# Kernel optimization log

Hardware: AMD Instinct MI355X
Metric: run time of the kernel (lower is better)

## Reference

```python
import jax, jax.numpy as jnp
import numpy as np

N, E, De, Dv = 40000, 8000, 32, 8   # nodes, hyperedges, edge degree, node degree
D, Q, EIG, VOC, NC = 256, 256, 64, 1000, 40  # vertex/edge dim, query dim, eig dim, centrality vocab, classes
LN_EPS = 1e-5


def _linear(x, W, b):
    return x @ W + b


def _layernorm(x, g, b):
    mu = jnp.mean(x, axis=-1, keepdims=True)
    var = jnp.mean(jnp.square(x - mu), axis=-1, keepdims=True)
    return (x - mu) * jax.lax.rsqrt(var + LN_EPS) * g + b


def setup_inputs() -> dict:
    key = jax.random.key(0)
    ks = iter(jax.random.split(key, 64))
    def nrm(shape, s=0.02):
        return (jax.random.normal(next(ks), shape, jnp.float32) * s).astype(jnp.float32)
    inp = {
        'vfeat': jax.random.normal(next(ks), (N, D), jnp.float32),
        'efeat': jax.random.normal(next(ks), (E, D), jnp.float32),
        'eign_vec': jax.random.normal(next(ks), (N, EIG), jnp.float32),
        'feat_v_gcn': jax.random.normal(next(ks), (N, D), jnp.float32),
        'cent1': jax.random.uniform(next(ks), (E, De), jnp.float32),
        'cent2': jax.random.uniform(next(ks), (N, Dv), jnp.float32),
        'cent_idx': jax.random.randint(next(ks), (N,), 0, VOC),
        'uniq_idx': jax.random.randint(next(ks), (N,), 0, VOC),
        'edge2node': jax.random.randint(next(ks), (E, De), 0, N),
        'node2edge': jax.random.randint(next(ks), (N, Dv), 0, E),
        # learned parameters (W: [in, out])
        'W_vtx': nrm((D, D)), 'b_vtx': jnp.zeros((D,), jnp.float32),
        'W_pe': nrm((EIG, D)), 'b_pe': jnp.zeros((D,), jnp.float32),
        'cs_emb': nrm((VOC, D)), 'un_emb': nrm((VOC, D)),
        'W_kv': nrm((D, Q)), 'b_kv': jnp.zeros((Q,), jnp.float32),
        'W_vv': nrm((D, D)), 'b_vv': jnp.zeros((D,), jnp.float32),
        'W_qe': nrm((D, Q)), 'b_qe': jnp.zeros((Q,), jnp.float32),
        'W_ke': nrm((D, Q)), 'b_ke': jnp.zeros((Q,), jnp.float32),
        'W_ve': nrm((D, D)), 'b_ve': jnp.zeros((D,), jnp.float32),
        'W_qv': nrm((D, Q)), 'b_qv': jnp.zeros((Q,), jnp.float32),
        'W_l1': nrm((D, Q)), 'b_l1': jnp.zeros((Q,), jnp.float32),
        'W_l2': nrm((Q, D)), 'b_l2': jnp.zeros((D,), jnp.float32),
        'W_l3': nrm((D, Q)), 'b_l3': jnp.zeros((Q,), jnp.float32),
        'W_l4': nrm((Q, D)), 'b_l4': jnp.zeros((D,), jnp.float32),
        'ln1_g': jnp.ones((D,), jnp.float32), 'ln1_b': jnp.zeros((D,), jnp.float32),
        'ln2_g': jnp.ones((D,), jnp.float32), 'ln2_b': jnp.zeros((D,), jnp.float32),
        'W_cls': nrm((D, NC)), 'b_cls': jnp.zeros((NC,), jnp.float32),
    }
    return inp


def _forward(vfeat, efeat, eign_vec, feat_v_gcn, cent1, cent2,
             W_vtx, b_vtx, W_pe, b_pe, cs_emb, un_emb,
             W_kv, b_kv, W_vv, b_vv, W_qe, b_qe, W_ke, b_ke, W_ve, b_ve, W_qv, b_qv,
             W_l1, b_l1, W_l2, b_l2, W_l3, b_l3, W_l4, b_l4,
             ln1_g, ln1_b, ln2_g, ln2_b, W_cls, b_cls,
             cent_idx, uniq_idx, edge2node, node2edge):
    scale = 1.0 / np.sqrt(float(W_kv.shape[1]))  # 1/sqrt(query_dim)
    # first_layer feature assembly: vtx_lin_1layer + PE + GCN + centrality/uniqueness embeddings
    feat_v = (_linear(vfeat, W_vtx, b_vtx) + _linear(eign_vec, W_pe, b_pe)
              + feat_v_gcn + cs_emb[cent_idx] + un_emb[uniq_idx])
    feat_e = efeat

    # ---- stage 1: hyperedges attend over member nodes ('in' etype) ----
    k_n = _linear(feat_v, W_kv, b_kv)              # [N,Q]
    v_n = _linear(feat_v, W_vv, b_vv)              # [N,D]
    q_e = _linear(feat_e, W_qe, b_qe)              # [E,Q]
    km = k_n[edge2node]                            # [E,De,Q]
    attn = jax.nn.leaky_relu(jnp.einsum('edq,eq->ed', km, q_e), 0.01) * scale
    score = jax.nn.softmax(attn + cent1, axis=1)   # centrality-biased softmax (k-core + clustering)
    h_e = jnp.einsum('ed,edc->ec', score, v_n[edge2node])  # [E,D]
    x_e = _layernorm(h_e + feat_e, ln1_g, ln1_b)
    f_e = _linear(jax.nn.relu(_linear(x_e, W_l1, b_l1)), W_l2, b_l2)
    feat_e = _layernorm(f_e + x_e, ln1_g, ln1_b)

    # ---- stage 2: nodes attend over incident hyperedges ('con' etype) ----
    k_e = _linear(feat_e, W_ke, b_ke)              # [E,Q]
    v_e = _linear(feat_e, W_ve, b_ve)              # [E,D]
    q_v = _linear(feat_v, W_qv, b_qv)              # [N,Q]
    km2 = k_e[node2edge]                           # [N,Dv,Q]
    attn2 = jax.nn.leaky_relu(jnp.einsum('ndq,nq->nd', km2, q_v), 0.01) * scale
    score2 = jax.nn.softmax(attn2 + cent2, axis=1)
    h_v = jnp.einsum('nd,ndc->nc', score2, v_e[node2edge])  # [N,D]
    x_v = _layernorm(h_v + feat_v, ln2_g, ln2_b)
    f_v = _linear(jax.nn.relu(_linear(x_v, W_l3, b_l3)), W_l4, b_l4)
    feat_v = _layernorm(f_v + x_v, ln2_g, ln2_b)

    # last_layer classification head (dropout is identity in eval)
    return _linear(feat_v, W_cls, b_cls)           # [N,NC]


def reference(vfeat, efeat, eign_vec, feat_v_gcn, cent1, cent2,
              cent_idx, uniq_idx, edge2node, node2edge,
              W_vtx, b_vtx, W_pe, b_pe, cs_emb, un_emb,
              W_kv, b_kv, W_vv, b_vv, W_qe, b_qe, W_ke, b_ke, W_ve, b_ve, W_qv, b_qv,
              W_l1, b_l1, W_l2, b_l2, W_l3, b_l3, W_l4, b_l4,
              ln1_g, ln1_b, ln2_g, ln2_b, W_cls, b_cls):
    return _forward(vfeat, efeat, eign_vec, feat_v_gcn, cent1, cent2,
                    W_vtx, b_vtx, W_pe, b_pe, cs_emb, un_emb,
                    W_kv, b_kv, W_vv, b_vv, W_qe, b_qe, W_ke, b_ke, W_ve, b_ve, W_qv, b_qv,
                    W_l1, b_l1, W_l2, b_l2, W_l3, b_l3, W_l4, b_l4,
                    ln1_g, ln1_b, ln2_g, ln2_b, W_cls, b_cls,
                    cent_idx, uniq_idx, edge2node, node2edge)
```

## Files before the change

kernel.cpp:

```cpp
#include <hip/hip_runtime.h>
#include <hip/hip_bf16.h>
#include <cstddef>

#define N_NODES 40000
#define N_EDGES 8000
#define DE 32
#define DV 8
#define DIM 256
#define QDIM 256
#define EIGD 64
#define NCLS 40
#define LN_EPS 1e-5f
#define ATT_SCALE 0.0625f

typedef unsigned short u16;
typedef unsigned int u32;
using i16x8 = __attribute__((ext_vector_type(8))) short;
using f32x4 = __attribute__((ext_vector_type(4))) float;

__device__ inline u16 f2b(float f) {
    union { float f; u32 u; } c; c.f = f;
    u32 u = c.u + 0x7FFF + ((c.u >> 16) & 1);
    return (u16)(u >> 16);
}
__device__ inline float b2f(u16 b) {
    union { u32 u; float f; } c; c.u = (u32)b << 16;
    return c.f;
}

__device__ inline void gload_lds16(const u16* g, u16* l) {
    __builtin_amdgcn_global_load_lds(
        (const __attribute__((address_space(1))) void*)g,
        (__attribute__((address_space(3))) void*)l, 16, 0, 0);
}

#define VMCNT10 asm volatile("s_waitcnt vmcnt(10)" ::: "memory")
#define VMCNT6  asm volatile("s_waitcnt vmcnt(6)" ::: "memory")
#define VMCNT0  asm volatile("s_waitcnt vmcnt(0)" ::: "memory")
#define LGKM0   asm volatile("s_waitcnt lgkmcnt(0)" ::: "memory")

__global__ __launch_bounds__(256) void cast_all(
    const float* __restrict__ vfeat, const float* __restrict__ eign,
    const float* __restrict__ efeat,
    u16* __restrict__ Vb, u16* __restrict__ Gb, u16* __restrict__ Eb)
{
    const int A4 = N_NODES * DIM / 4;
    const int B4 = N_NODES * EIGD / 4;
    const int C4 = N_EDGES * DIM / 4;
    const int tot = A4 + B4 + C4;
    for (int i = blockIdx.x * 256 + threadIdx.x; i < tot; i += gridDim.x * 256) {
        const float4* s; ushort4* d; int j;
        if (i < A4)            { s = (const float4*)vfeat; d = (ushort4*)Vb; j = i; }
        else if (i < A4 + B4)  { s = (const float4*)eign;  d = (ushort4*)Gb; j = i - A4; }
        else                   { s = (const float4*)efeat; d = (ushort4*)Eb; j = i - A4 - B4; }
        float4 v = s[j];
        ushort4 o;
        o.x = f2b(v.x); o.y = f2b(v.y); o.z = f2b(v.z); o.w = f2b(v.w);
        d[j] = o;
    }
}

__global__ __launch_bounds__(256) void prep_weights(
    const float* w0, const float* w1, const float* w2, const float* w3,
    const float* w4, const float* w5, const float* w6, const float* w7,
    const float* w8, const float* w9, const float* w10, const float* w11,
    const float* w12, u16* __restrict__ pool)
{
    const float* srcs[13] = {w0,w1,w2,w3,w4,w5,w6,w7,w8,w9,w10,w11,w12};
    const int Ks[13]  = {256,64,256,256,256,256,256,256,256,256,256,256,256};
    const int Nds[13] = {256,256,256,256,256,256,256,256,256,256,256,256,40};
    const int id = blockIdx.z;
    const float* W = srcs[id];
    u16* Wt = pool + (size_t)id * 65536;
    const int K = Ks[id], Nd = Nds[id];
    const int k0 = blockIdx.x * 32, n0 = blockIdx.y * 32;
    if (k0 >= K || n0 >= Nd) return;

    __shared__ float tile[32][33];
    const int x = threadIdx.x & 31, y4 = (threadIdx.x >> 5) * 4;
#pragma unroll
    for (int j = 0; j < 4; j++) {
        int k = k0 + y4 + j;
        tile[y4 + j][x] = (k < K && (n0 + x) < Nd) ? W[(size_t)k * Nd + n0 + x] : 0.f;
    }
    __syncthreads();
#pragma unroll
    for (int j = 0; j < 4; j++) {
        int n = n0 + y4 + j;
        if (n < Nd && (k0 + x) < K)
            Wt[(size_t)n * K + k0 + x] = f2b(tile[x][y4 + j]);
    }
}

template <int EPI, bool DUAL>
__global__ __launch_bounds__(256) void gemm_mfma(
    const u16* __restrict__ A, const u16* __restrict__ A2,
    const u16* __restrict__ Wt, const u16* __restrict__ Wt2,
    const float* __restrict__ bias0, const float* __restrict__ bias1,
    const float* __restrict__ bias2,
    const float* __restrict__ gcn, const float* __restrict__ emb1,
    const float* __restrict__ emb2, const int* __restrict__ idx1,
    const int* __restrict__ idx2,
    void* __restrict__ Cv, int M, int K1, int Ktot, int Nd)
{
    __shared__ u16 Asm[2][64 * 64];
    __shared__ u16 Bsm[2][128 * 64];
    const int t = threadIdx.x;
    const int lane = t & 63, w = t >> 6;
    const int wr = w >> 1, wc = w & 1;
    const int row0 = blockIdx.y * 64, col0 = blockIdx.x * 128;

    f32x4 acc[2][4] = {};

    const int srow = lane >> 3;
    const int sblk = ((lane & 7) ^ srow) * 8;

    const int fr = lane & 15, h = lane >> 4;
    const int lsw = fr & 7;
    const int nt = Ktot >> 6;

    auto stage = [&](int buf, int kt) {
        const int k0 = kt << 6;
        const bool first = !DUAL || (k0 < K1);
#pragma unroll
        for (int i = 0; i < 2; i++) {
            int r = w * 16 + i * 8;
            const u16* gp = first
                ? A  + (size_t)(row0 + r + srow) * K1 + k0 + sblk
                : A2 + (size_t)(row0 + r + srow) * 64 + (k0 - K1) + sblk;
            gload_lds16(gp, &Asm[buf][r * 64]);
        }
#pragma unroll
        for (int i = 0; i < 4; i++) {
            int r = w * 32 + i * 8;
            int ng = col0 + r + srow; if (ng > Nd - 1) ng = Nd - 1;
            const u16* gp = first
                ? Wt  + (size_t)ng * K1 + k0 + sblk
                : Wt2 + (size_t)ng * 64 + (k0 - K1) + sblk;
            gload_lds16(gp, &Bsm[buf][r * 64]);
        }
    };

    stage(0, 0);
    for (int kt = 0; kt < nt; ++kt) {
        const int cur = kt & 1;
        const bool more = (kt + 1 < nt);
        if (more) stage(cur ^ 1, kt + 1);
        if (more) { VMCNT6; } else { VMCNT0; }
        __builtin_amdgcn_s_barrier();

        i16x8 af[2][2], bf[2][4];
#pragma unroll
        for (int kk = 0; kk < 2; kk++) {
#pragma unroll
            for (int m = 0; m < 2; m++)
                af[kk][m] = *(const i16x8*)&Asm[cur][(wr * 32 + m * 16 + fr) * 64 +
                                                    ((kk * 4 + h) ^ lsw) * 8];
#pragma unroll
            for (int n = 0; n < 4; n++)
                bf[kk][n] = *(const i16x8*)&Bsm[cur][(wc * 64 + n * 16 + fr) * 64 +
                                                    ((kk * 4 + h) ^ lsw) * 8];
        }
        LGKM0;
        __builtin_amdgcn_sched_barrier(0);
        __builtin_amdgcn_s_barrier();

#pragma unroll
        for (int kk = 0; kk < 2; kk++)
#pragma unroll
            for (int m = 0; m < 2; m++)
#pragma unroll
                for (int n = 0; n < 4; n++)
                    acc[m][n] = __builtin_amdgcn_mfma_f32_16x16x32_bf16(
                        af[kk][m], bf[kk][n], acc[m][n], 0, 0, 0);
    }

#pragma unroll
    for (int m = 0; m < 2; m++) {
#pragma unroll
        for (int j = 0; j < 4; j++) {
            const int grow = row0 + wr * 32 + m * 16 + h * 4 + j;
            int i1 = 0, i2 = 0;
            if constexpr (EPI == 3) { i1 = idx1[grow]; i2 = idx2[grow]; }
#pragma unroll
            for (int n = 0; n < 4; n++) {
                const int gcol = col0 + wc * 64 + n * 16 + fr;
                if (EPI == 4 && gcol >= Nd) continue;
                float v;
                if constexpr (EPI == 3) {
                    v = acc[m][n][j] + bias0[gcol] + bias1[gcol];
                    v += gcn[(size_t)grow * Nd + gcol];
                    v += emb1[(size_t)i1 * Nd + gcol];
                    v += emb2[(size_t)i2 * Nd + gcol];
                } else {
                    const float* bp = (gcol < 256) ? bias0
                                     : ((gcol < 512) ? bias1 : bias2);
                    v = acc[m][n][j] + bp[gcol & 255];
                }
                if constexpr (EPI == 1) v = fmaxf(v, 0.f);
                if constexpr (EPI == 4)
                    ((float*)Cv)[(size_t)grow * Nd + gcol] = v;
                else
                    ((u16*)Cv)[(size_t)grow * Nd + gcol] = f2b(v);
            }
        }
    }
}

__global__ __launch_bounds__(256) void gemm_ln(
    const u16* __restrict__ A, const u16* __restrict__ Wt,
    const float* __restrict__ bias, const u16* __restrict__ resid,
    const float* __restrict__ g, const float* __restrict__ bb,
    u16* __restrict__ Y, int M)
{
    __shared__ u16 Asm[2][64 * 64];
    __shared__ u16 Bsm[2][256 * 64];
    const int t = threadIdx.x;
    const int lane = t & 63, w = t >> 6;
    const int row0 = blockIdx.y * 64;

    f32x4 acc[4][4] = {};

    const int srow = lane >> 3;
    const int sblk = ((lane & 7) ^ srow) * 8;
    const int fr = lane & 15, h = lane >> 4;
    const int lsw = fr & 7;

    auto stage = [&](int buf, int kt) {
        const int k0 = kt << 6;
#pragma unroll
        for (int i = 0; i < 2; i++) {
            int r = w * 16 + i * 8;
            gload_lds16(A + (size_t)(row0 + r + srow) * 256 + k0 + sblk,
                        &Asm[buf][r * 64]);
        }
#pragma unroll
        for (int i = 0; i < 8; i++) {
            int r = w * 64 + i * 8;
            gload_lds16(Wt + (size_t)(r + srow) * 256 + k0 + sblk,
                        &Bsm[buf][r * 64]);
        }
    };

    stage(0, 0);
    for (int kt = 0; kt < 4; ++kt) {
        const int cur = kt & 1;
        const bool more = (kt < 3);
        if (more) stage(cur ^ 1, kt + 1);
        if (more) { VMCNT10; } else { VMCNT0; }
        __builtin_amdgcn_s_barrier();

        i16x8 af[2][4], bf[2][4];
#pragma unroll
        for (int kk = 0; kk < 2; kk++) {
#pragma unroll
            for (int m = 0; m < 4; m++)
                af[kk][m] = *(const i16x8*)&Asm[cur][(m * 16 + fr) * 64 +
                                                    ((kk * 4 + h) ^ lsw) * 8];
#pragma unroll
            for (int n = 0; n < 4; n++)
                bf[kk][n] = *(const i16x8*)&Bsm[cur][(w * 64 + n * 16 + fr) * 64 +
                                                    ((kk * 4 + h) ^ lsw) * 8];
        }
        LGKM0;
        __builtin_amdgcn_sched_barrier(0);
        __builtin_amdgcn_s_barrier();

#pragma unroll
        for (int kk = 0; kk < 2; kk++)
#pragma unroll
            for (int m = 0; m < 4; m++)
#pragma unroll
                for (int n = 0; n < 4; n++)
                    acc[m][n] = __builtin_amdgcn_mfma_f32_16x16x32_bf16(
                        af[kk][m], bf[kk][n], acc[m][n], 0, 0, 0);
    }

    float* redS = (float*)&Asm[0][0];
    float* redQ = redS + 256;
#pragma unroll
    for (int m = 0; m < 4; m++) {
#pragma unroll
        for (int j = 0; j < 4; j++) {
            const int grow = row0 + m * 16 + h * 4 + j;
            float s = 0.f, q = 0.f;
#pragma unroll
            for (int n = 0; n < 4; n++) {
                const int gcol = w * 64 + n * 16 + fr;
                float v = acc[m][n][j] + bias[gcol] +
                          b2f(resid[(size_t)grow * 256 + gcol]);
                acc[m][n][j] = v;
                s += v; q += v * v;
            }
#pragma unroll
            for (int off = 1; off < 16; off <<= 1) {
                s += __shfl_xor(s, off, 64);
                q += __shfl_xor(q, off, 64);
            }
            if (fr == 0) {
                redS[(m * 16 + h * 4 + j) * 4 + w] = s;
                redQ[(m * 16 + h * 4 + j) * 4 + w] = q;
            }
        }
    }
    __syncthreads();
#pragma unroll
    for (int m = 0; m < 4; m++) {
#pragma unroll
        for (int j = 0; j < 4; j++) {
            const int r = m * 16 + h * 4 + j;
            const int grow = row0 + r;
            float4 s4 = *(const float4*)&redS[r * 4];
            float4 q4 = *(const float4*)&redQ[r * 4];
            float mu = (s4.x + s4.y + s4.z + s4.w) * (1.f / DIM);
            float var = (q4.x + q4.y + q4.z + q4.w) * (1.f / DIM) - mu * mu;
            float rr = rsqrtf(var + LN_EPS);
#pragma unroll
            for (int n = 0; n < 4; n++) {
                const int gcol = w * 64 + n * 16 + fr;
                float y = (acc[m][n][j] - mu) * rr * g[gcol] + bb[gcol];
                Y[(size_t)grow * 256 + gcol] = f2b(y);
            }
        }
    }
}

__global__ __launch_bounds__(256) void edge_attn(
    const u16* __restrict__ KVQn, const u16* __restrict__ QE,
    const float* __restrict__ efeat,
    const int* __restrict__ e2n, const float* __restrict__ cent1,
    const float* __restrict__ g, const float* __restrict__ bb,
    u16* __restrict__ XE)
{
    const int lane = threadIdx.x & 63, w = threadIdx.x >> 6;
    const int e = blockIdx.x * 4 + w;
    const int c4 = lane * 4;

    ushort4 q4 = *(const ushort4*)&QE[(size_t)e * QDIM + c4];
    const float q0 = b2f(q4.x), q1 = b2f(q4.y), q2 = b2f(q4.z), q3 = b2f(q4.w);

    int rows[DE];
#pragma unroll
    for (int d = 0; d < DE; d++) rows[d] = e2n[(size_t)e * DE + d];

    float m = -1e30f, l = 0.f;
    float a0 = 0.f, a1 = 0.f, a2 = 0.f, a3 = 0.f;
#pragma unroll
    for (int d0 = 0; d0 < DE; d0 += 4) {
        ushort4 k4[4], v4[4]; float p[4];
#pragma unroll
        for (int j = 0; j < 4; j++) {
            const u16* base = KVQn + (size_t)rows[d0 + j] * 768 + c4;
            k4[j] = *(const ushort4*)base;
            v4[j] = *(const ushort4*)(base + 256);
        }
#pragma unroll
        for (int j = 0; j < 4; j++)
            p[j] = q0 * b2f(k4[j].x) + q1 * b2f(k4[j].y)
                 + q2 * b2f(k4[j].z) + q3 * b2f(k4[j].w);
#pragma unroll
        for (int off = 32; off; off >>= 1)
#pragma unroll
            for (int j = 0; j < 4; j++) p[j] += __shfl_xor(p[j], off, 64);
#pragma unroll
        for (int j = 0; j < 4; j++) {
            float s = p[j];
            s = (s > 0.f ? s : 0.01f * s) * ATT_SCALE + cent1[(size_t)e * DE + d0 + j];
            float wgt;
            if (s > m) {
                float f = __expf(m - s);
                a0 *= f; a1 *= f; a2 *= f; a3 *= f; l *= f;
                m = s; wgt = 1.f;
            } else {
                wgt = __expf(s - m);
            }
            l += wgt;
            a0 = fmaf(wgt, b2f(v4[j].x), a0);
            a1 = fmaf(wgt, b2f(v4[j].y), a1);
            a2 = fmaf(wgt, b2f(v4[j].z), a2);
            a3 = fmaf(wgt, b2f(v4[j].w), a3);
        }
    }
    const float inv = 1.f / l;
    float4 ef = *(const float4*)&efeat[(size_t)e * DIM + c4];
    float x0 = a0 * inv + ef.x, x1 = a1 * inv + ef.y;
    float x2 = a2 * inv + ef.z, x3 = a3 * inv + ef.w;

    float mu = x0 + x1 + x2 + x3;
#pragma unroll
    for (int off = 32; off; off >>= 1) mu += __shfl_xor(mu, off, 64);
    mu *= (1.f / DIM);
    float d0_ = x0 - mu, d1 = x1 - mu, d2 = x2 - mu, d3 = x3 - mu;
    float var = d0_ * d0_ + d1 * d1 + d2 * d2 + d3 * d3;
#pragma unroll
    for (int off = 32; off; off >>= 1) var += __shfl_xor(var, off, 64);
    var *= (1.f / DIM);
    float r = rsqrtf(var + LN_EPS);
    float4 gv = *(const float4*)&g[c4];
    float4 bv = *(const float4*)&bb[c4];
    ushort4 o;
    o.x = f2b(d0_ * r * gv.x + bv.x); o.y = f2b(d1 * r * gv.y + bv.y);
    o.z = f2b(d2 * r * gv.z + bv.z); o.w = f2b(d3 * r * gv.w + bv.w);
    *(ushort4*)&XE[(size_t)e * DIM + c4] = o;
}

__global__ __launch_bounds__(256) void node_attn(
    const u16* __restrict__ KVe, const u16* __restrict__ KVQn,
    const u16* __restrict__ FV,
    const int* __restrict__ n2e, const float* __restrict__ cent2,
    const float* __restrict__ g, const float* __restrict__ bb,
    u16* __restrict__ XV)
{
    const int lane = threadIdx.x & 63, w = threadIdx.x >> 6;
    const int n = blockIdx.x * 4 + w;
    const int c4 = lane * 4;

    ushort4 q4 = *(const ushort4*)&KVQn[(size_t)n * 768 + 512 + c4];
    const float q0 = b2f(q4.x), q1 = b2f(q4.y), q2 = b2f(q4.z), q3 = b2f(q4.w);

    int rows[DV];
#pragma unroll
    for (int d = 0; d < DV; d++) rows[d] = n2e[(size_t)n * DV + d];

    ushort4 k4[DV], v4[DV];
#pragma unroll
    for (int d = 0; d < DV; d++) {
        const u16* base = KVe + (size_t)rows[d] * 512 + c4;
        k4[d] = *(const ushort4*)base;
        v4[d] = *(const ushort4*)(base + 256);
    }
    float p[DV];
#pragma unroll
    for (int d = 0; d < DV; d++)
        p[d] = q0 * b2f(k4[d].x) + q1 * b2f(k4[d].y)
             + q2 * b2f(k4[d].z) + q3 * b2f(k4[d].w);
#pragma unroll
    for (int off = 32; off; off >>= 1)
#pragma unroll
        for (int d = 0; d < DV; d++) p[d] += __shfl_xor(p[d], off, 64);

#pragma unroll
    for (int d = 0; d < DV; d++)
        p[d] = (p[d] > 0.f ? p[d] : 0.01f * p[d]) * ATT_SCALE
             + cent2[(size_t)n * DV + d];
    float mx = p[0];
#pragma unroll
    for (int d = 1; d < DV; d++) mx = fmaxf(mx, p[d]);
    float s = 0.f;
#pragma unroll
    for (int d = 0; d < DV; d++) { p[d] = __expf(p[d] - mx); s += p[d]; }
    const float inv = 1.f / s;

    float a0 = 0.f, a1 = 0.f, a2 = 0.f, a3 = 0.f;
#pragma unroll
    for (int d = 0; d < DV; d++) {
        float sd = p[d] * inv;
        a0 = fmaf(sd, b2f(v4[d].x), a0); a1 = fmaf(sd, b2f(v4[d].y), a1);
        a2 = fmaf(sd, b2f(v4[d].z), a2); a3 = fmaf(sd, b2f(v4[d].w), a3);
    }
    ushort4 f4 = *(const ushort4*)&FV[(size_t)n * DIM + c4];
    float x0 = a0 + b2f(f4.x), x1 = a1 + b2f(f4.y);
    float x2 = a2 + b2f(f4.z), x3 = a3 + b2f(f4.w);

    float mu = x0 + x1 + x2 + x3;
#pragma unroll
    for (int off = 32; off; off >>= 1) mu += __shfl_xor(mu, off, 64);
    mu *= (1.f / DIM);
    float d0 = x0 - mu, d1 = x1 - mu, d2 = x2 - mu, d3 = x3 - mu;
    float var = d0 * d0 + d1 * d1 + d2 * d2 + d3 * d3;
#pragma unroll
    for (int off = 32; off; off >>= 1) var += __shfl_xor(var, off, 64);
    var *= (1.f / DIM);
    float r = rsqrtf(var + LN_EPS);
    float4 gv = *(const float4*)&g[c4];
    float4 bv = *(const float4*)&bb[c4];
    ushort4 o;
    o.x = f2b(d0 * r * gv.x + bv.x); o.y = f2b(d1 * r * gv.y + bv.y);
    o.z = f2b(d2 * r * gv.z + bv.z); o.w = f2b(d3 * r * gv.w + bv.w);
    *(ushort4*)&XV[(size_t)n * DIM + c4] = o;
}

extern "C" void kernel_launch(void* const* d_in, const int* in_sizes, int n_in,
                              void* d_out, int out_size, void* d_ws, size_t ws_size,
                              hipStream_t stream)
{
    const float* vfeat  = (const float*)d_in[0];
    const float* efeat  = (const float*)d_in[1];
    const float* eign   = (const float*)d_in[2];
    const float* gcn    = (const float*)d_in[3];
    const float* cent1  = (const float*)d_in[4];
    const float* cent2  = (const float*)d_in[5];
    const int*   cidx   = (const int*)d_in[6];
    const int*   uidx   = (const int*)d_in[7];
    const int*   e2n    = (const int*)d_in[8];
    const int*   n2e    = (const int*)d_in[9];
    const float* W_vtx  = (const float*)d_in[10]; const float* b_vtx = (const float*)d_in[11];
    const float* W_pe   = (const float*)d_in[12]; const float* b_pe  = (const float*)d_in[13];
    const float* cs_emb = (const float*)d_in[14]; const float* un_emb= (const float*)d_in[15];
    const float* W_kv   = (const float*)d_in[16]; const float* b_kv  = (const float*)d_in[17];
    const float* W_vv   = (const float*)d_in[18]; const float* b_vv  = (const float*)d_in[19];
    const float* W_qe   = (const float*)d_in[20]; const float* b_qe  = (const float*)d_in[21];
    const float* W_ke   = (const float*)d_in[22]; const float* b_ke  = (const float*)d_in[23];
    const float* W_ve   = (const float*)d_in[24]; const float* b_ve  = (const float*)d_in[25];
    const float* W_qv   = (const float*)d_in[26]; const float* b_qv  = (const float*)d_in[27];
    const float* W_l1   = (const float*)d_in[28]; const float* b_l1  = (const float*)d_in[29];
    const float* W_l2   = (const float*)d_in[30]; const float* b_l2  = (const float*)d_in[31];
    const float* W_l3   = (const float*)d_in[32]; const float* b_l3  = (const float*)d_in[33];
    const float* W_l4   = (const float*)d_in[34]; const float* b_l4  = (const float*)d_in[35];
    const float* ln1_g  = (const float*)d_in[36]; const float* ln1_b = (const float*)d_in[37];
    const float* ln2_g  = (const float*)d_in[38]; const float* ln2_b = (const float*)d_in[39];
    const float* W_cls  = (const float*)d_in[40]; const float* b_cls = (const float*)d_in[41];
    float* out = (float*)d_out;

    const size_t NE = (size_t)N_NODES * DIM;
    const size_t EE = (size_t)N_EDGES * DIM;
    u16* ws = (u16*)d_ws;
    u16* FVb  = ws;
    u16* Vb   = FVb + NE;
    u16* Gb   = Vb + NE;
    u16* KVQn = Gb + NE / 4;
    u16* B2   = KVQn + 3 * NE;
    u16* Eb   = B2 + NE;
    u16* QEb  = Eb + EE;
    u16* XE   = QEb + EE;
    u16* FE   = XE + EE;
    u16* KVe  = FE + EE;
    u16* Wp   = KVe + 2 * EE;
    u16* Wt_vtx = Wp +  0 * 65536;
    u16* Wt_pe  = Wp +  1 * 65536;
    u16* Wt_kvq = Wp +  2 * 65536;
    u16* Wt_qe  = Wp +  5 * 65536;
    u16* Wt_kve = Wp +  6 * 65536;
    u16* Wt_l1  = Wp +  8 * 65536;
    u16* Wt_l2  = Wp +  9 * 65536;
    u16* Wt_l3  = Wp + 10 * 65536;
    u16* Wt_l4  = Wp + 11 * 65536;
    u16* Wt_cls = Wp + 12 * 65536;
    u16* T0 = Vb;
    u16* TE = Eb;

    const dim3 blk(256);
    const dim3 gW(8, 8, 13);
    const dim3 gA(2, N_NODES / 64);
    const dim3 gKVQ(6, N_NODES / 64);
    const dim3 gQE(2, N_EDGES / 64);
    const dim3 gL1(2, N_EDGES / 64);
    const dim3 gLN_E(1, N_EDGES / 64);
    const dim3 gKVe(4, N_EDGES / 64);
    const dim3 gL3(2, N_NODES / 64);
    const dim3 gLN_N(1, N_NODES / 64);
    const dim3 gCl(1, N_NODES / 64);

    prep_weights<<<gW, blk, 0, stream>>>(
        W_vtx, W_pe, W_kv, W_vv, W_qv, W_qe, W_ke, W_ve,
        W_l1, W_l2, W_l3, W_l4, W_cls, Wp);
    cast_all<<<2048, blk, 0, stream>>>(vfeat, eign, efeat, Vb, Gb, Eb);

    gemm_mfma<3, true><<<gA, blk, 0, stream>>>(Vb, Gb, Wt_vtx, Wt_pe,
        b_vtx, b_pe, nullptr, gcn, cs_emb, un_emb, cidx, uidx,
        FVb, N_NODES, 256, 320, DIM);

    gemm_mfma<0, false><<<gKVQ, blk, 0, stream>>>(FVb, nullptr, Wt_kvq, nullptr,
        b_kv, b_vv, b_qv, nullptr, nullptr, nullptr, nullptr, nullptr,
        KVQn, N_NODES, 256, 256, 768);
    gemm_mfma<0, false><<<gQE, blk, 0, stream>>>(Eb, nullptr, Wt_qe, nullptr,
        b_qe, nullptr, nullptr, nullptr, nullptr, nullptr, nullptr, nullptr,
        QEb, N_EDGES, 256, 256, QDIM);
    edge_attn<<<N_EDGES / 4, blk, 0, stream>>>(KVQn, QEb, efeat, e2n, cent1,
        ln1_g, ln1_b, XE);
    gemm_mfma<1, false><<<gL1, blk, 0, stream>>>(XE, nullptr, Wt_l1, nullptr,
        b_l1, nullptr, nullptr, nullptr, nullptr, nullptr, nullptr, nullptr,
        TE, N_EDGES, 256, 256, QDIM);
    gemm_ln<<<gLN_E, blk, 0, stream>>>(TE, Wt_l2, b_l2, XE, ln1_g, ln1_b,
        FE, N_EDGES);

    gemm_mfma<0, false><<<gKVe, blk, 0, stream>>>(FE, nullptr, Wt_kve, nullptr,
        b_ke, b_ve, nullptr, nullptr, nullptr, nullptr, nullptr, nullptr,
        KVe, N_EDGES, 256, 256, 512);
    node_attn<<<N_NODES / 4, blk, 0, stream>>>(KVe, KVQn, FVb, n2e, cent2,
        ln2_g, ln2_b, B2);
    gemm_mfma<1, false><<<gL3, blk, 0, stream>>>(B2, nullptr, Wt_l3, nullptr,
        b_l3, nullptr, nullptr, nullptr, nullptr, nullptr, nullptr, nullptr,
        T0, N_NODES, 256, 256, QDIM);
    gemm_ln<<<gLN_N, blk, 0, stream>>>(T0, Wt_l4, b_l4, B2, ln2_g, ln2_b,
        FVb, N_NODES);

    gemm_mfma<4, false><<<gCl, blk, 0, stream>>>(FVb, nullptr, Wt_cls, nullptr,
        b_cls, nullptr, nullptr, nullptr, nullptr, nullptr, nullptr, nullptr,
        out, N_NODES, 256, 256, NCLS);
}
```

Baseline: 264.3 us.

## Unify GEMMs into 64x256 tile kernel with fused fp32 input cast

Removes the standalone fp32-to-bf16 cast kernel. GEMMs now read fp32 vfeat/eign/efeat directly and convert them into LDS inside the staging step. All GEMMs move to a single 64x256-tile template that also absorbs the LayerNorm epilogue, and the classifier GEMM idles warps past column 40. The edge and node attention kernels are restructured: node_attn handles two nodes per wave with half the blocks, and edge_attn preloads its gather indices. This saves an extra HBM round trip and launch, in exchange for larger tiles with fewer blocks and VGPR-staged conversion of A, which may hurt latency hiding.

```diff
diff --git a/kernel.cpp b/kernel.cpp
--- a/kernel.cpp
+++ b/kernel.cpp
@@ -34,31 +34,8 @@
         (__attribute__((address_space(3))) void*)l, 16, 0, 0);
 }
 
-#define VMCNT10 asm volatile("s_waitcnt vmcnt(10)" ::: "memory")
-#define VMCNT6  asm volatile("s_waitcnt vmcnt(6)" ::: "memory")
 #define VMCNT0  asm volatile("s_waitcnt vmcnt(0)" ::: "memory")
 #define LGKM0   asm volatile("s_waitcnt lgkmcnt(0)" ::: "memory")
-
-__global__ __launch_bounds__(256) void cast_all(
-    const float* __restrict__ vfeat, const float* __restrict__ eign,
-    const float* __restrict__ efeat,
-    u16* __restrict__ Vb, u16* __restrict__ Gb, u16* __restrict__ Eb)
-{
-    const int A4 = N_NODES * DIM / 4;
-    const int B4 = N_NODES * EIGD / 4;
-    const int C4 = N_EDGES * DIM / 4;
-    const int tot = A4 + B4 + C4;
-    for (int i = blockIdx.x * 256 + threadIdx.x; i < tot; i += gridDim.x * 256) {
-        const float4* s; ushort4* d; int j;
-        if (i < A4)            { s = (const float4*)vfeat; d = (ushort4*)Vb; j = i; }
-        else if (i < A4 + B4)  { s = (const float4*)eign;  d = (ushort4*)Gb; j = i - A4; }
-        else                   { s = (const float4*)efeat; d = (ushort4*)Eb; j = i - A4 - B4; }
-        float4 v = s[j];
-        ushort4 o;
-        o.x = f2b(v.x); o.y = f2b(v.y); o.z = f2b(v.z); o.w = f2b(v.w);
-        d[j] = o;
-    }
-}
 
 __global__ __launch_bounds__(256) void prep_weights(
     const float* w0, const float* w1, const float* w2, const float* w3,
@@ -92,52 +69,78 @@
     }
 }
 
-template <int EPI, bool DUAL>
-__global__ __launch_bounds__(256) void gemm_mfma(
-    const u16* __restrict__ A, const u16* __restrict__ A2,
+template <int EPI, int AMODE>
+__global__ __launch_bounds__(256) void gemm256(
+    const void* __restrict__ Av, const float* __restrict__ A2,
     const u16* __restrict__ Wt, const u16* __restrict__ Wt2,
     const float* __restrict__ bias0, const float* __restrict__ bias1,
-    const float* __restrict__ bias2,
+    const float* __restrict__ bias2, const u16* __restrict__ resid,
     const float* __restrict__ gcn, const float* __restrict__ emb1,
     const float* __restrict__ emb2, const int* __restrict__ idx1,
-    const int* __restrict__ idx2,
-    void* __restrict__ Cv, int M, int K1, int Ktot, int Nd)
+    const int* __restrict__ idx2, const float* __restrict__ lng,
+    const float* __restrict__ lnb,
+    void* __restrict__ Cv, int M, int Nd, int nt)
 {
     __shared__ u16 Asm[2][64 * 64];
-    __shared__ u16 Bsm[2][128 * 64];
+    __shared__ u16 Bsm[2][256 * 64];
     const int t = threadIdx.x;
     const int lane = t & 63, w = t >> 6;
-    const int wr = w >> 1, wc = w & 1;
-    const int row0 = blockIdx.y * 64, col0 = blockIdx.x * 128;
-
-    f32x4 acc[2][4] = {};
+    const int row0 = blockIdx.y * 64, col0 = blockIdx.x * 256;
+
+    f32x4 acc[4][4] = {};
 
     const int srow = lane >> 3;
-    const int sblk = ((lane & 7) ^ srow) * 8;
-
+    const int sblk8 = ((lane & 7) ^ srow) * 8;
+    const int dblk8 = (lane & 7) * 8;
     const int fr = lane & 15, h = lane >> 4;
     const int lsw = fr & 7;
-    const int nt = Ktot >> 6;
+    const bool wactive = (EPI != 4) || (w * 64 < Nd);
 
     auto stage = [&](int buf, int kt) {
         const int k0 = kt << 6;
-        const bool first = !DUAL || (k0 < K1);
-#pragma unroll
-        for (int i = 0; i < 2; i++) {
-            int r = w * 16 + i * 8;
-            const u16* gp = first
-                ? A  + (size_t)(row0 + r + srow) * K1 + k0 + sblk
-                : A2 + (size_t)(row0 + r + srow) * 64 + (k0 - K1) + sblk;
-            gload_lds16(gp, &Asm[buf][r * 64]);
-        }
-#pragma unroll
-        for (int i = 0; i < 4; i++) {
-            int r = w * 32 + i * 8;
-            int ng = col0 + r + srow; if (ng > Nd - 1) ng = Nd - 1;
-            const u16* gp = first
-                ? Wt  + (size_t)ng * K1 + k0 + sblk
-                : Wt2 + (size_t)ng * 64 + (k0 - K1) + sblk;
-            gload_lds16(gp, &Bsm[buf][r * 64]);
+        const bool tail = (AMODE == 2) && (k0 >= 256);
+        if constexpr (AMODE == 0) {
+#pragma unroll
+            for (int i = 0; i < 2; i++) {
+                const int r = w * 16 + i * 8;
+                gload_lds16((const u16*)Av + (size_t)(row0 + r + srow) * 256 + k0 + sblk8,
+                            &Asm[buf][r * 64]);
+            }
+#pragma unroll
+            for (int i = 0; i < 8; i++) {
+                const int r = w * 64 + i * 8;
+                int ng = col0 + r + srow; if (ng > Nd - 1) ng = Nd - 1;
+                gload_lds16(Wt + (size_t)ng * 256 + k0 + sblk8, &Bsm[buf][r * 64]);
+            }
+        } else {
+            float4 fa[2][2];
+#pragma unroll
+            for (int i = 0; i < 2; i++) {
+                const int r = w * 16 + i * 8;
+                const float* ap = tail
+                    ? A2 + (size_t)(row0 + r + srow) * 64 + sblk8
+                    : (const float*)Av + (size_t)(row0 + r + srow) * 256 + k0 + sblk8;
+                fa[i][0] = *(const float4*)ap;
+                fa[i][1] = *(const float4*)(ap + 4);
+            }
+#pragma unroll
+            for (int i = 0; i < 8; i++) {
+                const int r = w * 64 + i * 8;
+                int ng = col0 + r + srow; if (ng > Nd - 1) ng = Nd - 1;
+                const u16* gp = tail ? Wt2 + (size_t)ng * 64 + sblk8
+                                     : Wt + (size_t)ng * 256 + k0 + sblk8;
+                gload_lds16(gp, &Bsm[buf][r * 64]);
+            }
+#pragma unroll
+            for (int i = 0; i < 2; i++) {
+                const int r = w * 16 + i * 8;
+                i16x8 v;
+                v[0] = (short)f2b(fa[i][0].x); v[1] = (short)f2b(fa[i][0].y);
+                v[2] = (short)f2b(fa[i][0].z); v[3] = (short)f2b(fa[i][0].w);
+                v[4] = (short)f2b(fa[i][1].x); v[5] = (short)f2b(fa[i][1].y);
+                v[6] = (short)f2b(fa[i][1].z); v[7] = (short)f2b(fa[i][1].w);
+                *(i16x8*)&Asm[buf][(r + srow) * 64 + dblk8] = v;
+            }
         }
     };
 
@@ -146,180 +149,119 @@
         const int cur = kt & 1;
         const bool more = (kt + 1 < nt);
         if (more) stage(cur ^ 1, kt + 1);
-        if (more) { VMCNT6; } else { VMCNT0; }
+        if (more) {
+            if constexpr (AMODE == 0) asm volatile("s_waitcnt vmcnt(10)" ::: "memory");
+            else                      asm volatile("s_waitcnt vmcnt(8)" ::: "memory");
+        } else { VMCNT0; }
         __builtin_amdgcn_s_barrier();
 
-        i16x8 af[2][2], bf[2][4];
-#pragma unroll
-        for (int kk = 0; kk < 2; kk++) {
-#pragma unroll
-            for (int m = 0; m < 2; m++)
-                af[kk][m] = *(const i16x8*)&Asm[cur][(wr * 32 + m * 16 + fr) * 64 +
-                                                    ((kk * 4 + h) ^ lsw) * 8];
-#pragma unroll
-            for (int n = 0; n < 4; n++)
-                bf[kk][n] = *(const i16x8*)&Bsm[cur][(wc * 64 + n * 16 + fr) * 64 +
-                                                    ((kk * 4 + h) ^ lsw) * 8];
+        i16x8 af[2][4], bfr[2][4];
+        if (wactive) {
+#pragma unroll
+            for (int kk = 0; kk < 2; kk++) {
+#pragma unroll
+                for (int m = 0; m < 4; m++)
+                    af[kk][m] = *(const i16x8*)&Asm[cur][(m * 16 + fr) * 64 +
+                                                        ((kk * 4 + h) ^ lsw) * 8];
+#pragma unroll
+                for (int n = 0; n < 4; n++)
+                    bfr[kk][n] = *(const i16x8*)&Bsm[cur][(w * 64 + n * 16 + fr) * 64 +
+                                                         ((kk * 4 + h) ^ lsw) * 8];
+            }
         }
         LGKM0;
         __builtin_amdgcn_sched_barrier(0);
         __builtin_amdgcn_s_barrier();
 
-#pragma unroll
-        for (int kk = 0; kk < 2; kk++)
-#pragma unroll
-            for (int m = 0; m < 2; m++)
-#pragma unroll
-                for (int n = 0; n < 4; n++)
-                    acc[m][n] = __builtin_amdgcn_mfma_f32_16x16x32_bf16(
-                        af[kk][m], bf[kk][n], acc[m][n], 0, 0, 0);
-    }
-
-#pragma unroll
-    for (int m = 0; m < 2; m++) {
-#pragma unroll
-        for (int j = 0; j < 4; j++) {
-            const int grow = row0 + wr * 32 + m * 16 + h * 4 + j;
-            int i1 = 0, i2 = 0;
-            if constexpr (EPI == 3) { i1 = idx1[grow]; i2 = idx2[grow]; }
-#pragma unroll
-            for (int n = 0; n < 4; n++) {
-                const int gcol = col0 + wc * 64 + n * 16 + fr;
-                if (EPI == 4 && gcol >= Nd) continue;
-                float v;
-                if constexpr (EPI == 3) {
-                    v = acc[m][n][j] + bias0[gcol] + bias1[gcol];
-                    v += gcn[(size_t)grow * Nd + gcol];
-                    v += emb1[(size_t)i1 * Nd + gcol];
-                    v += emb2[(size_t)i2 * Nd + gcol];
-                } else {
-                    const float* bp = (gcol < 256) ? bias0
-                                     : ((gcol < 512) ? bias1 : bias2);
-                    v = acc[m][n][j] + bp[gcol & 255];
+        if (wactive) {
+#pragma unroll
+            for (int kk = 0; kk < 2; kk++)
+#pragma unroll
+                for (int m = 0; m < 4; m++)
+#pragma unroll
+                    for (int n = 0; n < 4; n++)
+                        acc[m][n] = __builtin_amdgcn_mfma_f32_16x16x32_bf16(
+                            af[kk][m], bfr[kk][n], acc[m][n], 0, 0, 0);
+        }
+    }
+
+    if constexpr (EPI == 5) {
+        float* redS = (float*)&Asm[0][0];
+        float* redQ = redS + 256;
+#pragma unroll
+        for (int m = 0; m < 4; m++) {
+#pragma unroll
+            for (int j = 0; j < 4; j++) {
+                const int grow = row0 + m * 16 + h * 4 + j;
+                float s = 0.f, q = 0.f;
+#pragma unroll
+                for (int n = 0; n < 4; n++) {
+                    const int gcol = w * 64 + n * 16 + fr;
+                    float v = acc[m][n][j] + bias0[gcol] +
+                              b2f(resid[(size_t)grow * 256 + gcol]);
+                    acc[m][n][j] = v;
+                    s += v; q += v * v;
                 }
-                if constexpr (EPI == 1) v = fmaxf(v, 0.f);
-                if constexpr (EPI == 4)
-                    ((float*)Cv)[(size_t)grow * Nd + gcol] = v;
-                else
-                    ((u16*)Cv)[(size_t)grow * Nd + gcol] = f2b(v);
-            }
-        }
-    }
-}
-
-__global__ __launch_bounds__(256) void gemm_ln(
-    const u16* __restrict__ A, const u16* __restrict__ Wt,
-    const float* __restrict__ bias, const u16* __restrict__ resid,
-    const float* __restrict__ g, const float* __restrict__ bb,
-    u16* __restrict__ Y, int M)
-{
-    __shared__ u16 Asm[2][64 * 64];
-    __shared__ u16 Bsm[2][256 * 64];
-    const int t = threadIdx.x;
-    const int lane = t & 63, w = t >> 6;
-    const int row0 = blockIdx.y * 64;
-
-    f32x4 acc[4][4] = {};
-
-    const int srow = lane >> 3;
-    const int sblk = ((lane & 7) ^ srow) * 8;
-    const int fr = lane & 15, h = lane >> 4;
-    const int lsw = fr & 7;
-
-    auto stage = [&](int buf, int kt) {
-        const int k0 = kt << 6;
-#pragma unroll
-        for (int i = 0; i < 2; i++) {
-            int r = w * 16 + i * 8;
-            gload_lds16(A + (size_t)(row0 + r + srow) * 256 + k0 + sblk,
-                        &Asm[buf][r * 64]);
-        }
-#pragma unroll
-        for (int i = 0; i < 8; i++) {
-            int r = w * 64 + i * 8;
-            gload_lds16(Wt + (size_t)(r + srow) * 256 + k0 + sblk,
-                        &Bsm[buf][r * 64]);
-        }
-    };
-
-    stage(0, 0);
-    for (int kt = 0; kt < 4; ++kt) {
-        const int cur = kt & 1;
-        const bool more = (kt < 3);
-        if (more) stage(cur ^ 1, kt + 1);
-        if (more) { VMCNT10; } else { VMCNT0; }
-        __builtin_amdgcn_s_barrier();
-
-        i16x8 af[2][4], bf[2][4];
-#pragma unroll
-        for (int kk = 0; kk < 2; kk++) {
-#pragma unroll
-            for (int m = 0; m < 4; m++)
-                af[kk][m] = *(const i16x8*)&Asm[cur][(m * 16 + fr) * 64 +
-                                                    ((kk * 4 + h) ^ lsw) * 8];
-#pragma unroll
-            for (int n = 0; n < 4; n++)
-                bf[kk][n] = *(const i16x8*)&Bsm[cur][(w * 64 + n * 16 + fr) * 64 +
-                                                    ((kk * 4 + h) ^ lsw) * 8];
-        }
-        LGKM0;
-        __builtin_amdgcn_sched_barrier(0);
-        __builtin_amdgcn_s_barrier();
-
-#pragma unroll
-        for (int kk = 0; kk < 2; kk++)
-#pragma unroll
-            for (int m = 0; m < 4; m++)
-#pragma unroll
-                for (int n = 0; n < 4; n++)
-                    acc[m][n] = __builtin_amdgcn_mfma_f32_16x16x32_bf16(
-                        af[kk][m], bf[kk][n], acc[m][n], 0, 0, 0);
-    }
-
-    float* redS = (float*)&Asm[0][0];
-    float* redQ = redS + 256;
-#pragma unroll
-    for (int m = 0; m < 4; m++) {
-#pragma unroll
-        for (int j = 0; j < 4; j++) {
-            const int grow = row0 + m * 16 + h * 4 + j;
-            float s = 0.f, q = 0.f;
-#pragma unroll
-            for (int n = 0; n < 4; n++) {
-                const int gcol = w * 64 + n * 16 + fr;
-                float v = acc[m][n][j] + bias[gcol] +
-                          b2f(resid[(size_t)grow * 256 + gcol]);
-                acc[m][n][j] = v;
-                s += v; q += v * v;
-            }
-#pragma unroll
-            for (int off = 1; off < 16; off <<= 1) {
-                s += __shfl_xor(s, off, 64);
-                q += __shfl_xor(q, off, 64);
-            }
-            if (fr == 0) {
-                redS[(m * 16 + h * 4 + j) * 4 + w] = s;
-                redQ[(m * 16 + h * 4 + j) * 4 + w] = q;
-            }
-        }
-    }
-    __syncthreads();
-#pragma unroll
-    for (int m = 0; m < 4; m++) {
-#pragma unroll
-        for (int j = 0; j < 4; j++) {
-            const int r = m * 16 + h * 4 + j;
-            const int grow = row0 + r;
-            float4 s4 = *(const float4*)&redS[r * 4];
-            float4 q4 = *(const float4*)&redQ[r * 4];
-            float mu = (s4.x + s4.y + s4.z + s4.w) * (1.f / DIM);
-            float var = (q4.x + q4.y + q4.z + q4.w) * (1.f / DIM) - mu * mu;
-            float rr = rsqrtf(var + LN_EPS);
-#pragma unroll
-            for (int n = 0; n < 4; n++) {
-                const int gcol = w * 64 + n * 16 + fr;
-                float y = (acc[m][n][j] - mu) * rr * g[gcol] + bb[gcol];
-                Y[(size_t)grow * 256 + gcol] = f2b(y);
+#pragma unroll
+                for (int off = 1; off < 16; off <<= 1) {
+                    s += __shfl_xor(s, off, 64);
+                    q += __shfl_xor(q, off, 64);
+                }
+                if (fr == 0) {
+                    redS[(m * 16 + h * 4 + j) * 4 + w] = s;
+                    redQ[(m * 16 + h * 4 + j) * 4 + w] = q;
+                }
+            }
+        }
+        __syncthreads();
+#pragma unroll
+        for (int m = 0; m < 4; m++) {
+#pragma unroll
+            for (int j = 0; j < 4; j++) {
+                const int r = m * 16 + h * 4 + j;
+                const int grow = row0 + r;
+                float4 s4 = *(const float4*)&redS[r * 4];
+                float4 q4 = *(const float4*)&redQ[r * 4];
+                float mu = (s4.x + s4.y + s4.z + s4.w) * (1.f / DIM);
+                float var = (q4.x + q4.y + q4.z + q4.w) * (1.f / DIM) - mu * mu;
+                float rr = rsqrtf(var + LN_EPS);
+#pragma unroll
+                for (int n = 0; n < 4; n++) {
+                    const int gcol = w * 64 + n * 16 + fr;
+                    float y = (acc[m][n][j] - mu) * rr * lng[gcol] + lnb[gcol];
+                    ((u16*)Cv)[(size_t)grow * 256 + gcol] = f2b(y);
+                }
+            }
+        }
+    } else {
+        if (!wactive) return;
+        const float* bp = (col0 == 0) ? bias0 : ((col0 == 256) ? bias1 : bias2);
+#pragma unroll
+        for (int m = 0; m < 4; m++) {
+#pragma unroll
+            for (int j = 0; j < 4; j++) {
+                const int grow = row0 + m * 16 + h * 4 + j;
+                int i1 = 0, i2 = 0;
+                if constexpr (EPI == 3) { i1 = idx1[grow]; i2 = idx2[grow]; }
+#pragma unroll
+                for (int n = 0; n < 4; n++) {
+                    const int gcol = col0 + w * 64 + n * 16 + fr;
+                    if (EPI == 4 && gcol >= Nd) continue;
+                    float v;
+                    if constexpr (EPI == 3) {
+                        v = acc[m][n][j] + bias0[gcol] + bias1[gcol];
+                        v += gcn[(size_t)grow * 256 + gcol];
+                        v += emb1[(size_t)i1 * 256 + gcol];
+                        v += emb2[(size_t)i2 * 256 + gcol];
+                    } else {
+                        v = acc[m][n][j] + bp[gcol - col0];
+                    }
+                    if constexpr (EPI == 1) v = fmaxf(v, 0.f);
+                    if constexpr (EPI == 4)
+                        ((float*)Cv)[(size_t)grow * Nd + gcol] = v;
+                    else
+                        ((u16*)Cv)[(size_t)grow * Nd + gcol] = f2b(v);
+                }
             }
         }
     }
@@ -339,59 +281,82 @@
     ushort4 q4 = *(const ushort4*)&QE[(size_t)e * QDIM + c4];
     const float q0 = b2f(q4.x), q1 = b2f(q4.y), q2 = b2f(q4.z), q3 = b2f(q4.w);
 
+    int4 rv[8];
+#pragma unroll
+    for (int i = 0; i < 8; i++)
+        rv[i] = *(const int4*)&e2n[(size_t)e * DE + i * 4];
     int rows[DE];
 #pragma unroll
-    for (int d = 0; d < DE; d++) rows[d] = e2n[(size_t)e * DE + d];
-
-    float m = -1e30f, l = 0.f;
+    for (int i = 0; i < 8; i++) {
+        rows[i * 4 + 0] = rv[i].x; rows[i * 4 + 1] = rv[i].y;
+        rows[i * 4 + 2] = rv[i].z; rows[i * 4 + 3] = rv[i].w;
+    }
+
+    float p[DE];
+#pragma unroll
+    for (int g0 = 0; g0 < DE; g0 += 16) {
+        ushort4 k4[16];
+#pragma unroll
+        for (int j = 0; j < 16; j++)
+            k4[j] = *(const ushort4*)&KVQn[(size_t)rows[g0 + j] * 768 + c4];
+#pragma unroll
+        for (int j = 0; j < 16; j++)
+            p[g0 + j] = q0 * b2f(k4[j].x) + q1 * b2f(k4[j].y)
+                      + q2 * b2f(k4[j].z) + q3 * b2f(k4[j].w);
+    }
+#pragma unroll
+    for (int off = 32; off; off >>= 1)
+#pragma unroll
+        for (int d = 0; d < DE; d++)
+            p[d] += __shfl_xor(p[d], off, 64);
+
+    float4 cv[8];
+#pragma unroll
+    for (int i = 0; i < 8; i++)
+        cv[i] = *(const float4*)&cent1[(size_t)e * DE + i * 4];
+    float cent[DE];
+#pragma unroll
+    for (int i = 0; i < 8; i++) {
+        cent[i * 4 + 0] = cv[i].x; cent[i * 4 + 1] = cv[i].y;
+        cent[i * 4 + 2] = cv[i].z; cent[i * 4 + 3] = cv[i].w;
+    }
+#pragma unroll
+    for (int d = 0; d < DE; d++)
+        p[d] = (p[d] > 0.f ? p[d] : 0.01f * p[d]) * ATT_SCALE + cent[d];
+
+    float mx = p[0];
+#pragma unroll
+    for (int d = 1; d < DE; d++) mx = fmaxf(mx, p[d]);
+    float s = 0.f;
+#pragma unroll
+    for (int d = 0; d < DE; d++) { p[d] = __expf(p[d] - mx); s += p[d]; }
+    const float inv = 1.f / s;
+#pragma unroll
+    for (int d = 0; d < DE; d++) p[d] *= inv;
+
     float a0 = 0.f, a1 = 0.f, a2 = 0.f, a3 = 0.f;
 #pragma unroll
-    for (int d0 = 0; d0 < DE; d0 += 4) {
-        ushort4 k4[4], v4[4]; float p[4];
-#pragma unroll
-        for (int j = 0; j < 4; j++) {
-            const u16* base = KVQn + (size_t)rows[d0 + j] * 768 + c4;
-            k4[j] = *(const ushort4*)base;
-            v4[j] = *(const ushort4*)(base + 256);
-        }
-#pragma unroll
-        for (int j = 0; j < 4; j++)
-            p[j] = q0 * b2f(k4[j].x) + q1 * b2f(k4[j].y)
-                 + q2 * b2f(k4[j].z) + q3 * b2f(k4[j].w);
-#pragma unroll
-        for (int off = 32; off; off >>= 1)
-#pragma unroll
-            for (int j = 0; j < 4; j++) p[j] += __shfl_xor(p[j], off, 64);
-#pragma unroll
-        for (int j = 0; j < 4; j++) {
-            float s = p[j];
-            s = (s > 0.f ? s : 0.01f * s) * ATT_SCALE + cent1[(size_t)e * DE + d0 + j];
-            float wgt;
-            if (s > m) {
-                float f = __expf(m - s);
-                a0 *= f; a1 *= f; a2 *= f; a3 *= f; l *= f;
-                m = s; wgt = 1.f;
-            } else {
-                wgt = __expf(s - m);
-            }
-            l += wgt;
-            a0 = fmaf(wgt, b2f(v4[j].x), a0);
-            a1 = fmaf(wgt, b2f(v4[j].y), a1);
-            a2 = fmaf(wgt, b2f(v4[j].z), a2);
-            a3 = fmaf(wgt, b2f(v4[j].w), a3);
-        }
-    }
-    const float inv = 1.f / l;
+    for (int g0 = 0; g0 < DE; g0 += 16) {
+        ushort4 v4[16];
+#pragma unroll
+        for (int j = 0; j < 16; j++)
+            v4[j] = *(const ushort4*)&KVQn[(size_t)rows[g0 + j] * 768 + 256 + c4];
+#pragma unroll
+        for (int j = 0; j < 16; j++) {
+            const float sd = p[g0 + j];
+            a0 = fmaf(sd, b2f(v4[j].x), a0); a1 = fmaf(sd, b2f(v4[j].y), a1);
+            a2 = fmaf(sd, b2f(v4[j].z), a2); a3 = fmaf(sd, b2f(v4[j].w), a3);
+        }
+    }
     float4 ef = *(const float4*)&efeat[(size_t)e * DIM + c4];
-    float x0 = a0 * inv + ef.x, x1 = a1 * inv + ef.y;
-    float x2 = a2 * inv + ef.z, x3 = a3 * inv + ef.w;
+    float x0 = a0 + ef.x, x1 = a1 + ef.y, x2 = a2 + ef.z, x3 = a3 + ef.w;
 
     float mu = x0 + x1 + x2 + x3;
 #pragma unroll
     for (int off = 32; off; off >>= 1) mu += __shfl_xor(mu, off, 64);
     mu *= (1.f / DIM);
-    float d0_ = x0 - mu, d1 = x1 - mu, d2 = x2 - mu, d3 = x3 - mu;
-    float var = d0_ * d0_ + d1 * d1 + d2 * d2 + d3 * d3;
+    float d0 = x0 - mu, d1 = x1 - mu, d2 = x2 - mu, d3 = x3 - mu;
+    float var = d0 * d0 + d1 * d1 + d2 * d2 + d3 * d3;
 #pragma unroll
     for (int off = 32; off; off >>= 1) var += __shfl_xor(var, off, 64);
     var *= (1.f / DIM);
@@ -399,7 +364,7 @@
     float4 gv = *(const float4*)&g[c4];
     float4 bv = *(const float4*)&bb[c4];
     ushort4 o;
-    o.x = f2b(d0_ * r * gv.x + bv.x); o.y = f2b(d1 * r * gv.y + bv.y);
+    o.x = f2b(d0 * r * gv.x + bv.x); o.y = f2b(d1 * r * gv.y + bv.y);
     o.z = f2b(d2 * r * gv.z + bv.z); o.w = f2b(d3 * r * gv.w + bv.w);
     *(ushort4*)&XE[(size_t)e * DIM + c4] = o;
 }
@@ -412,72 +377,115 @@
     u16* __restrict__ XV)
 {
     const int lane = threadIdx.x & 63, w = threadIdx.x >> 6;
-    const int n = blockIdx.x * 4 + w;
+    const int na = blockIdx.x * 8 + w * 2, nb = na + 1;
     const int c4 = lane * 4;
 
-    ushort4 q4 = *(const ushort4*)&KVQn[(size_t)n * 768 + 512 + c4];
-    const float q0 = b2f(q4.x), q1 = b2f(q4.y), q2 = b2f(q4.z), q3 = b2f(q4.w);
-
-    int rows[DV];
-#pragma unroll
-    for (int d = 0; d < DV; d++) rows[d] = n2e[(size_t)n * DV + d];
-
-    ushort4 k4[DV], v4[DV];
+    ushort4 qa4 = *(const ushort4*)&KVQn[(size_t)na * 768 + 512 + c4];
+    ushort4 qb4 = *(const ushort4*)&KVQn[(size_t)nb * 768 + 512 + c4];
+    const float qa0 = b2f(qa4.x), qa1 = b2f(qa4.y), qa2 = b2f(qa4.z), qa3 = b2f(qa4.w);
+    const float qb0 = b2f(qb4.x), qb1 = b2f(qb4.y), qb2 = b2f(qb4.z), qb3 = b2f(qb4.w);
+
+    int4 r0 = *(const int4*)&n2e[(size_t)na * DV];
+    int4 r1 = *(const int4*)&n2e[(size_t)na * DV + 4];
+    int4 r2 = *(const int4*)&n2e[(size_t)nb * DV];
+    int4 r3 = *(const int4*)&n2e[(size_t)nb * DV + 4];
+    int rA[8] = {r0.x, r0.y, r0.z, r0.w, r1.x, r1.y, r1.z, r1.w};
+    int rB[8] = {r2.x, r2.y, r2.z, r2.w, r3.x, r3.y, r3.z, r3.w};
+
+    ushort4 kA[8], vA[8], kB[8], vB[8];
 #pragma unroll
     for (int d = 0; d < DV; d++) {
-        const u16* base = KVe + (size_t)rows[d] * 512 + c4;
-        k4[d] = *(const ushort4*)base;
-        v4[d] = *(const ushort4*)(base + 256);
-    }
-    float p[DV];
-#pragma unroll
-    for (int d = 0; d < DV; d++)
-        p[d] = q0 * b2f(k4[d].x) + q1 * b2f(k4[d].y)
-             + q2 * b2f(k4[d].z) + q3 * b2f(k4[d].w);
-#pragma unroll
-    for (int off = 32; off; off >>= 1)
-#pragma unroll
-        for (int d = 0; d < DV; d++) p[d] += __shfl_xor(p[d], off, 64);
-
-#pragma unroll
-    for (int d = 0; d < DV; d++)
-        p[d] = (p[d] > 0.f ? p[d] : 0.01f * p[d]) * ATT_SCALE
-             + cent2[(size_t)n * DV + d];
-    float mx = p[0];
-#pragma unroll
-    for (int d = 1; d < DV; d++) mx = fmaxf(mx, p[d]);
-    float s = 0.f;
-#pragma unroll
-    for (int d = 0; d < DV; d++) { p[d] = __expf(p[d] - mx); s += p[d]; }
-    const float inv = 1.f / s;
+        const u16* b = KVe + (size_t)rA[d] * 512 + c4;
+        kA[d] = *(const ushort4*)b; vA[d] = *(const ushort4*)(b + 256);
+    }
+#pragma unroll
+    for (int d = 0; d < DV; d++) {
+        const u16* b = KVe + (size_t)rB[d] * 512 + c4;
+        kB[d] = *(const ushort4*)b; vB[d] = *(const ushort4*)(b + 256);
+    }
+
+    float pA[8], pB[8];
+#pragma unroll
+    for (int d = 0; d < DV; d++) {
+        pA[d] = qa0 * b2f(kA[d].x) + qa1 * b2f(kA[d].y)
+              + qa2 * b2f(kA[d].z) + qa3 * b2f(kA[d].w);
+        pB[d] = qb0 * b2f(kB[d].x) + qb1 * b2f(kB[d].y)
+              + qb2 * b2f(kB[d].z) + qb3 * b2f(kB[d].w);
+    }
+#pragma unroll
+    for (int off = 32; off; off >>= 1) {
+#pragma unroll
+        for (int d = 0; d < DV; d++) {
+            pA[d] += __shfl_xor(pA[d], off, 64);
+            pB[d] += __shfl_xor(pB[d], off, 64);
+        }
+    }
+    float4 cA0 = *(const float4*)&cent2[(size_t)na * DV];
+    float4 cA1 = *(const float4*)&cent2[(size_t)na * DV + 4];
+    float4 cB0 = *(const float4*)&cent2[(size_t)nb * DV];
+    float4 cB1 = *(const float4*)&cent2[(size_t)nb * DV + 4];
+    float cA[8] = {cA0.x, cA0.y, cA0.z, cA0.w, cA1.x, cA1.y, cA1.z, cA1.w};
+    float cB[8] = {cB0.x, cB0.y, cB0.z, cB0.w, cB1.x, cB1.y, cB1.z, cB1.w};
+#pragma unroll
+    for (int d = 0; d < DV; d++) {
+        pA[d] = (pA[d] > 0.f ? pA[d] : 0.01f * pA[d]) * ATT_SCALE + cA[d];
+        pB[d] = (pB[d] > 0.f ? pB[d] : 0.01f * pB[d]) * ATT_SCALE + cB[d];
+    }
+    float mA = pA[0], mB = pB[0];
+#pragma unroll
+    for (int d = 1; d < DV; d++) { mA = fmaxf(mA, pA[d]); mB = fmaxf(mB, pB[d]); }
+    float sA = 0.f, sB = 0.f;
+#pragma unroll
+    for (int d = 0; d < DV; d++) {
+        pA[d] = __expf(pA[d] - mA); sA += pA[d];
+        pB[d] = __expf(pB[d] - mB); sB += pB[d];
+    }
+    const float iA = 1.f / sA, iB = 1.f / sB;
 
     float a0 = 0.f, a1 = 0.f, a2 = 0.f, a3 = 0.f;
+    float b0 = 0.f, b1 = 0.f, b2 = 0.f, b3 = 0.f;
 #pragma unroll
     for (int d = 0; d < DV; d++) {
-        float sd = p[d] * inv;
-        a0 = fmaf(sd, b2f(v4[d].x), a0); a1 = fmaf(sd, b2f(v4[d].y), a1);
-        a2 = fmaf(sd, b2f(v4[d].z), a2); a3 = fmaf(sd, b2f(v4[d].w), a3);
-    }
-    ushort4 f4 = *(const ushort4*)&FV[(size_t)n * DIM + c4];
-    float x0 = a0 + b2f(f4.x), x1 = a1 + b2f(f4.y);
-    float x2 = a2 + b2f(f4.z), x3 = a3 + b2f(f4.w);
-
-    float mu = x0 + x1 + x2 + x3;
-#pragma unroll
-    for (int off = 32; off; off >>= 1) mu += __shfl_xor(mu, off, 64);
-    mu *= (1.f / DIM);
-    float d0 = x0 - mu, d1 = x1 - mu, d2 = x2 - mu, d3 = x3 - mu;
-    float var = d0 * d0 + d1 * d1 + d2 * d2 + d3 * d3;
-#pragma unroll
-    for (int off = 32; off; off >>= 1) var += __shfl_xor(var, off, 64);
-    var *= (1.f / DIM);
-    float r = rsqrtf(var + LN_EPS);
+        const float sa = pA[d] * iA, sb = pB[d] * iB;
+        a0 = fmaf(sa, b2f(vA[d].x), a0); a1 = fmaf(sa, b2f(vA[d].y), a1);
+        a2 = fmaf(sa, b2f(vA[d].z), a2); a3 = fmaf(sa, b2f(vA[d].w), a3);
+        b0 = fmaf(sb, b2f(vB[d].x), b0); b1 = fmaf(sb, b2f(vB[d].y), b1);
+        b2 = fmaf(sb, b2f(vB[d].z), b2); b3 = fmaf(sb, b2f(vB[d].w), b3);
+    }
+    ushort4 fa = *(const ushort4*)&FV[(size_t)na * DIM + c4];
+    ushort4 fb = *(const ushort4*)&FV[(size_t)nb * DIM + c4];
+    float xa0 = a0 + b2f(fa.x), xa1 = a1 + b2f(fa.y);
+    float xa2 = a2 + b2f(fa.z), xa3 = a3 + b2f(fa.w);
+    float xb0 = b0 + b2f(fb.x), xb1 = b1 + b2f(fb.y);
+    float xb2 = b2 + b2f(fb.z), xb3 = b3 + b2f(fb.w);
+
+    float muA = xa0 + xa1 + xa2 + xa3, muB = xb0 + xb1 + xb2 + xb3;
+#pragma unroll
+    for (int off = 32; off; off >>= 1) {
+        muA += __shfl_xor(muA, off, 64);
+        muB += __shfl_xor(muB, off, 64);
+    }
+    muA *= (1.f / DIM); muB *= (1.f / DIM);
+    float da0 = xa0 - muA, da1 = xa1 - muA, da2 = xa2 - muA, da3 = xa3 - muA;
+    float db0 = xb0 - muB, db1 = xb1 - muB, db2 = xb2 - muB, db3 = xb3 - muB;
+    float vA_ = da0 * da0 + da1 * da1 + da2 * da2 + da3 * da3;
+    float vB_ = db0 * db0 + db1 * db1 + db2 * db2 + db3 * db3;
+#pragma unroll
+    for (int off = 32; off; off >>= 1) {
+        vA_ += __shfl_xor(vA_, off, 64);
+        vB_ += __shfl_xor(vB_, off, 64);
+    }
+    const float rA_ = rsqrtf(vA_ * (1.f / DIM) + LN_EPS);
+    const float rB_ = rsqrtf(vB_ * (1.f / DIM) + LN_EPS);
     float4 gv = *(const float4*)&g[c4];
     float4 bv = *(const float4*)&bb[c4];
-    ushort4 o;
-    o.x = f2b(d0 * r * gv.x + bv.x); o.y = f2b(d1 * r * gv.y + bv.y);
-    o.z = f2b(d2 * r * gv.z + bv.z); o.w = f2b(d3 * r * gv.w + bv.w);
-    *(ushort4*)&XV[(size_t)n * DIM + c4] = o;
+    ushort4 oa, ob;
+    oa.x = f2b(da0 * rA_ * gv.x + bv.x); oa.y = f2b(da1 * rA_ * gv.y + bv.y);
+    oa.z = f2b(da2 * rA_ * gv.z + bv.z); oa.w = f2b(da3 * rA_ * gv.w + bv.w);
+    ob.x = f2b(db0 * rB_ * gv.x + bv.x); ob.y = f2b(db1 * rB_ * gv.y + bv.y);
+    ob.z = f2b(db2 * rB_ * gv.z + bv.z); ob.w = f2b(db3 * rB_ * gv.w + bv.w);
+    *(ushort4*)&XV[(size_t)na * DIM + c4] = oa;
+    *(ushort4*)&XV[(size_t)nb * DIM + c4] = ob;
 }
 
 extern "C" void kernel_launch(void* const* d_in, const int* in_sizes, int n_in,
@@ -516,14 +524,13 @@
     const size_t EE = (size_t)N_EDGES * DIM;
     u16* ws = (u16*)d_ws;
     u16* FVb  = ws;
-    u16* Vb   = FVb + NE;
-    u16* Gb   = Vb + NE;
-    u16* KVQn = Gb + NE / 4;
+    u16* KVQn = FVb + NE;
     u16* B2   = KVQn + 3 * NE;
-    u16* Eb   = B2 + NE;
-    u16* QEb  = Eb + EE;
+    u16* T0   = B2 + NE;
+    u16* QEb  = T0 + NE;
     u16* XE   = QEb + EE;
-    u16* FE   = XE + EE;
+    u16* TE   = XE + EE;
+    u16* FE   = TE + EE;
     u16* KVe  = FE + EE;
     u16* Wp   = KVe + 2 * EE;
     u16* Wt_vtx = Wp +  0 * 65536;
@@ -536,56 +543,50 @@
     u16* Wt_l3  = Wp + 10 * 65536;
     u16* Wt_l4  = Wp + 11 * 65536;
     u16* Wt_cls = Wp + 12 * 65536;
-    u16* T0 = Vb;
-    u16* TE = Eb;
 
     const dim3 blk(256);
     const dim3 gW(8, 8, 13);
-    const dim3 gA(2, N_NODES / 64);
-    const dim3 gKVQ(6, N_NODES / 64);
-    const dim3 gQE(2, N_EDGES / 64);
-    const dim3 gL1(2, N_EDGES / 64);
-    const dim3 gLN_E(1, N_EDGES / 64);
-    const dim3 gKVe(4, N_EDGES / 64);
-    const dim3 gL3(2, N_NODES / 64);
-    const dim3 gLN_N(1, N_NODES / 64);
-    const dim3 gCl(1, N_NODES / 64);
+    const dim3 gN1(1, N_NODES / 64);
+    const dim3 gKVQ(3, N_NODES / 64);
+    const dim3 gE1(1, N_EDGES / 64);
+    const dim3 gKVe(2, N_EDGES / 64);
 
     prep_weights<<<gW, blk, 0, stream>>>(
         W_vtx, W_pe, W_kv, W_vv, W_qv, W_qe, W_ke, W_ve,
         W_l1, W_l2, W_l3, W_l4, W_cls, Wp);
-    cast_all<<<2048, blk, 0, stream>>>(vfeat, eign, efeat, Vb, Gb, Eb);
-
-    gemm_mfma<3, true><<<gA, blk, 0, stream>>>(Vb, Gb, Wt_vtx, Wt_pe,
-        b_vtx, b_pe, nullptr, gcn, cs_emb, un_emb, cidx, uidx,
-        FVb, N_NODES, 256, 320, DIM);
-
-    gemm_mfma<0, false><<<gKVQ, blk, 0, stream>>>(FVb, nullptr, Wt_kvq, nullptr,
-        b_kv, b_vv, b_qv, nullptr, nullptr, nullptr, nullptr, nullptr,
-        KVQn, N_NODES, 256, 256, 768);
-    gemm_mfma<0, false><<<gQE, blk, 0, stream>>>(Eb, nullptr, Wt_qe, nullptr,
-        b_qe, nullptr, nullptr, nullptr, nullptr, nullptr, nullptr, nullptr,
-        QEb, N_EDGES, 256, 256, QDIM);
+
+    gemm256<3, 2><<<gN1, blk, 0, stream>>>(vfeat, eign, Wt_vtx, Wt_pe,
+        b_vtx, b_pe, nullptr, nullptr, gcn, cs_emb, un_emb, cidx, uidx,
+        nullptr, nullptr, FVb, N_NODES, 256, 5);
+
+    gemm256<0, 0><<<gKVQ, blk, 0, stream>>>(FVb, nullptr, Wt_kvq, nullptr,
+        b_kv, b_vv, b_qv, nullptr, nullptr, nullptr, nullptr, nullptr, nullptr,
+        nullptr, nullptr, KVQn, N_NODES, 768, 4);
+    gemm256<0, 1><<<gE1, blk, 0, stream>>>(efeat, nullptr, Wt_qe, nullptr,
+        b_qe, nullptr, nullptr, nullptr, nullptr, nullptr, nullptr, nullptr, nullptr,
+        nullptr, nullptr, QEb, N_EDGES, 256, 4);
     edge_attn<<<N_EDGES / 4, blk, 0, stream>>>(KVQn, QEb, efeat, e2n, cent1,
         ln1_g, ln1_b, XE);
-    gemm_mfma<1, false><<<gL1, blk, 0, stream>>>(XE, nullptr, Wt_l1, nullptr,
-        b_l1, nullptr, nullptr, nullptr, nullptr, nullptr, nullptr, nullptr,
-        TE, N_EDGES, 256, 256, QDIM);
-    gemm_ln<<<gLN_E, blk, 0, stream>>>(TE, Wt_l2, b_l2, XE, ln1_g, ln1_b,
-        FE, N_EDGES);
-
-    gemm_mfma<0, false><<<gKVe, blk, 0, stream>>>(FE, nullptr, Wt_kve, nullptr,
-        b_ke, b_ve, nullptr, nullptr, nullptr, nullptr, nullptr, nullptr,
-        KVe, N_EDGES, 256, 256, 512);
-    node_attn<<<N_NODES / 4, blk, 0, stream>>>(KVe, KVQn, FVb, n2e, cent2,
+    gemm256<1, 0><<<gE1, blk, 0, stream>>>(XE, nullptr, Wt_l1, nullptr,
+        b_l1, nullptr, nullptr, nullptr, nullptr, nullptr, nullptr, nullptr, nullptr,
+        nullptr, nullptr, TE, N_EDGES, 256, 4);
+    gemm256<5, 0><<<gE1, blk, 0, stream>>>(TE, nullptr, Wt_l2, nullptr,
+        b_l2, nullptr, nullptr, XE, nullptr, nullptr, nullptr, nullptr, nullptr,
+        ln1_g, ln1_b, FE, N_EDGES, 256, 4);
+
+    gemm256<0, 0><<<gKVe, blk, 0, stream>>>(FE, nullptr, Wt_kve, nullptr,
+        b_ke, b_ve, nullptr, nullptr, nullptr, nullptr, nullptr, nullptr, nullptr,
+        nullptr, nullptr, KVe, N_EDGES, 512, 4);
+    node_attn<<<N_NODES / 8, blk, 0, stream>>>(KVe, KVQn, FVb, n2e, cent2,
         ln2_g, ln2_b, B2);
-    gemm_mfma<1, false><<<gL3, blk, 0, stream>>>(B2, nullptr, Wt_l3, nullptr,
-        b_l3, nullptr, nullptr, nullptr, nullptr, nullptr, nullptr, nullptr,
-        T0, N_NODES, 256, 256, QDIM);
-    gemm_ln<<<gLN_N, blk, 0, stream>>>(T0, Wt_l4, b_l4, B2, ln2_g, ln2_b,
-        FVb, N_NODES);
-
-    gemm_mfma<4, false><<<gCl, blk, 0, stream>>>(FVb, nullptr, Wt_cls, nullptr,
-        b_cls, nullptr, nullptr, nullptr, nullptr, nullptr, nullptr, nullptr,
-        out, N_NODES, 256, 256, NCLS);
-}
+    gemm256<1, 0><<<gN1, blk, 0, stream>>>(B2, nullptr, Wt_l3, nullptr,
+        b_l3, nullptr, nullptr, nullptr, nullptr, nullptr, nullptr, nullptr, nullptr,
+        nullptr, nullptr, T0, N_NODES, 256, 4);
+    gemm256<5, 0><<<gN1, blk, 0, stream>>>(T0, nullptr, Wt_l4, nullptr,
+        b_l4, nullptr, nullptr, B2, nullptr, nullptr, nullptr, nullptr, nullptr,
+        ln2_g, ln2_b, FVb, N_NODES, 256, 4);
+
+    gemm256<4, 0><<<gN1, blk, 0, stream>>>(FVb, nullptr, Wt_cls, nullptr,
+        b_cls, nullptr, nullptr, nullptr, nullptr, nullptr, nullptr, nullptr, nullptr,
+        nullptr, nullptr, out, N_NODES, NCLS, 4);
+}
```

New measurement: 269.3 us. About the same (+1.9%).
